# Kernel tuning notes

Measured on AMD Instinct MI355X. Metric: run time of the kernel, lower is better.

The kernel has to match this reference:

```python
import jax, jax.numpy as jnp
import numpy as np

ALPHA = 0.2  # LeakyReLU negative slope


def setup_inputs() -> dict:
    key = jax.random.key(0)
    ks = jax.random.split(key, 7)
    B, Wn, K, E, O = 16, 64, 256, 128, 64
    s = lambda k, shape, fan: jax.random.normal(k, shape, jnp.float32) * (1.0 / np.sqrt(fan))
    return {
        "x": jax.random.normal(ks[0], (B, Wn, K), jnp.float32),
        "lin_w": s(ks[1], (E, 2 * Wn), 2 * Wn),   # torch Linear weight (out,in)
        "lin_b": jnp.zeros((E,), jnp.float32),
        "a": s(ks[2], (E,), E),
        "bias_kk": s(ks[3], (K, K), K) * 0.1,
        "fc_w": s(ks[4], (O, K), K),
        "fc_b": jnp.zeros((O,), jnp.float32),
    }


def reference(x, lin_w, lin_b, a, bias_kk, fc_w, fc_b):
    # x: (B, W, K) -> v: (B, K, W); K nodes, W features per node
    v = jnp.transpose(x, (0, 2, 1))
    Wn = v.shape[-1]
    # lin(concat(v_i, v_j)) == v_i @ W1^T + v_j @ W2^T + b  (avoids O(K^2*2W) concat)
    W1, W2 = lin_w[:, :Wn], lin_w[:, Wn:]
    left = jnp.einsum("bkw,ew->bke", v, W1)   # (B,K,E)
    right = jnp.einsum("bkw,ew->bke", v, W2)  # (B,K,E)
    g = left[:, :, None, :] + right[:, None, :, :] + lin_b  # (B,K,K,E)
    g = jnp.where(g >= 0, g, ALPHA * g)  # LeakyReLU
    e = jnp.einsum("bije,e->bij", g, a) + bias_kk  # (B,K,K)
    attn = jax.nn.softmax(e, axis=2)
    # dropout p=0.0 / eval mode -> identity
    h = jax.nn.sigmoid(jnp.einsum("bij,bjw->biw", attn, v))  # (B,K,W)
    out = jnp.einsum("bwk,ok->bwo", jnp.transpose(h, (0, 2, 1)), fc_w) + fc_b
    return out  # (B, W, out_dim)
```

## Files before the change

kernel.cpp:

```cpp
#include <hip/hip_runtime.h>
#include <hip/hip_bf16.h>

#define ALPHA 0.2f
#define C1 0.6f
#define C2 0.4f

__global__ __launch_bounds__(256) void k_proj(
    const float* __restrict__ x, const float* __restrict__ lin_w,
    float* __restrict__ left, float* __restrict__ right, float* __restrict__ v) {
  const int b  = blockIdx.x >> 5;
  const int k0 = (blockIdx.x & 31) * 8;
  const int tid = threadIdx.x;

  __shared__ float s_x[8][68];

  {
    const int w  = tid >> 2;
    const int kq = tid & 3;
    float2 xv = *(const float2*)(x + b * 16384 + w * 256 + k0 + kq * 2);
    s_x[kq * 2 + 0][w] = xv.x;
    s_x[kq * 2 + 1][w] = xv.y;
  }
  __syncthreads();

  if (tid < 128) {
    const int k  = tid >> 4;
    const int wq = tid & 15;
    float4 vv = *(const float4*)&s_x[k][wq * 4];
    *(float4*)(v + (b * 256 + k0 + k) * 64 + wq * 4) = vv;
  }

  const int e  = tid & 127;
  const int kh = tid >> 7;
  float accL[4] = {0, 0, 0, 0};
  float accR[4] = {0, 0, 0, 0};
  const float4* w1 = (const float4*)(lin_w + e * 128);
  const float4* w2 = w1 + 16;
#pragma unroll
  for (int wc = 0; wc < 16; ++wc) {
    float4 l = w1[wc];
    float4 r = w2[wc];
#pragma unroll
    for (int k = 0; k < 4; ++k) {
      float4 sx = *(const float4*)&s_x[kh * 4 + k][wc * 4];
      accL[k] += sx.x * l.x + sx.y * l.y + sx.z * l.z + sx.w * l.w;
      accR[k] += sx.x * r.x + sx.y * r.y + sx.z * r.z + sx.w * r.w;
    }
  }
#pragma unroll
  for (int k = 0; k < 4; ++k) {
    int kk = (b * 256 + k0 + kh * 4 + k) * 128 + e;
    left[kk]  = accL[k];
    right[kk] = accR[k];
  }
}

__global__ __launch_bounds__(256) void k_attn(
    const float* __restrict__ left, const float* __restrict__ right,
    const float* __restrict__ lin_b, const float* __restrict__ a,
    const float* __restrict__ bias_kk, const float* __restrict__ v,
    float* __restrict__ h) {
  const int b   = blockIdx.x >> 5;
  const int i0  = (blockIdx.x & 31) * 8;
  const int tid = threadIdx.x;

  __shared__ float s_lb[8][132];
  __shared__ float s_a[128];
  __shared__ float s_ca[128];
  __shared__ float s_AL[8];
  __shared__ float s_sc[8][260];
  __shared__ float s_inv[8];
  __shared__ float s_v[128][68];

  float bk[8];
#pragma unroll
  for (int i = 0; i < 8; ++i) bk[i] = bias_kk[(i0 + i) * 256 + tid];

  if (tid < 128) {
    float av = a[tid];
    s_a[tid]  = av;
    s_ca[tid] = C2 * av;
  }
  {
    const int ii = tid >> 5;
    const int e4 = (tid & 31) * 4;
    float4 lv = *(const float4*)(left + (b * 256 + i0 + ii) * 128 + e4);
    float4 bv = *(const float4*)(lin_b + e4);
    lv.x += bv.x; lv.y += bv.y; lv.z += bv.z; lv.w += bv.w;
    *(float4*)&s_lb[ii][e4] = lv;
  }
  __syncthreads();

  {
    const int ii = tid >> 5, sl = tid & 31;
    float p = 0.f;
#pragma unroll
    for (int m = 0; m < 4; ++m) p += s_a[sl * 4 + m] * s_lb[ii][sl * 4 + m];
#pragma unroll
    for (int off = 16; off > 0; off >>= 1) p += __shfl_xor(p, off, 64);
    if (sl == 0) s_AL[ii] = p;
  }

  float acc[8];
#pragma unroll
  for (int i = 0; i < 8; ++i) acc[i] = 0.f;
  float ar = 0.f;
  const float4* rp = (const float4*)(right + (b * 256 + tid) * 128);
#pragma unroll
  for (int ec = 0; ec < 8; ++ec) {
    float4 r0 = rp[ec * 4 + 0], r1 = rp[ec * 4 + 1],
           r2 = rp[ec * 4 + 2], r3 = rp[ec * 4 + 3];
    float4 a0 = *(const float4*)&s_a[ec * 16 + 0];
    float4 a1 = *(const float4*)&s_a[ec * 16 + 4];
    float4 a2 = *(const float4*)&s_a[ec * 16 + 8];
    float4 a3 = *(const float4*)&s_a[ec * 16 + 12];
    ar += a0.x * r0.x + a0.y * r0.y + a0.z * r0.z + a0.w * r0.w;
    ar += a1.x * r1.x + a1.y * r1.y + a1.z * r1.z + a1.w * r1.w;
    ar += a2.x * r2.x + a2.y * r2.y + a2.z * r2.z + a2.w * r2.w;
    ar += a3.x * r3.x + a3.y * r3.y + a3.z * r3.z + a3.w * r3.w;
    float4 c0 = *(const float4*)&s_ca[ec * 16 + 0];
    float4 c1 = *(const float4*)&s_ca[ec * 16 + 4];
    float4 c2 = *(const float4*)&s_ca[ec * 16 + 8];
    float4 c3 = *(const float4*)&s_ca[ec * 16 + 12];
#pragma unroll
    for (int i = 0; i < 8; ++i) {
      float4 l0 = *(const float4*)&s_lb[i][ec * 16 + 0];
      float4 l1 = *(const float4*)&s_lb[i][ec * 16 + 4];
      float4 l2 = *(const float4*)&s_lb[i][ec * 16 + 8];
      float4 l3 = *(const float4*)&s_lb[i][ec * 16 + 12];
      float t, s = acc[i];
      t = l0.x + r0.x; s = fmaf(c0.x, fabsf(t), s);
      t = l0.y + r0.y; s = fmaf(c0.y, fabsf(t), s);
      t = l0.z + r0.z; s = fmaf(c0.z, fabsf(t), s);
      t = l0.w + r0.w; s = fmaf(c0.w, fabsf(t), s);
      t = l1.x + r1.x; s = fmaf(c1.x, fabsf(t), s);
      t = l1.y + r1.y; s = fmaf(c1.y, fabsf(t), s);
      t = l1.z + r1.z; s = fmaf(c1.z, fabsf(t), s);
      t = l1.w + r1.w; s = fmaf(c1.w, fabsf(t), s);
      t = l2.x + r2.x; s = fmaf(c2.x, fabsf(t), s);
      t = l2.y + r2.y; s = fmaf(c2.y, fabsf(t), s);
      t = l2.z + r2.z; s = fmaf(c2.z, fabsf(t), s);
      t = l2.w + r2.w; s = fmaf(c2.w, fabsf(t), s);
      t = l3.x + r3.x; s = fmaf(c3.x, fabsf(t), s);
      t = l3.y + r3.y; s = fmaf(c3.y, fabsf(t), s);
      t = l3.z + r3.z; s = fmaf(c3.z, fabsf(t), s);
      t = l3.w + r3.w; s = fmaf(c3.w, fabsf(t), s);
      acc[i] = s;
    }
  }
  __syncthreads();

#pragma unroll
  for (int i = 0; i < 8; ++i) {
    float sc = fmaf(C1, s_AL[i] + ar, acc[i]) + bk[i];
    s_sc[i][tid] = __expf(sc);
  }
  __syncthreads();

  {
    const int wv = tid >> 6, lane = tid & 63;
#pragma unroll
    for (int rr = 0; rr < 2; ++rr) {
      int i = wv * 2 + rr;
      float s = s_sc[i][lane] + s_sc[i][lane + 64] +
                s_sc[i][lane + 128] + s_sc[i][lane + 192];
#pragma unroll
      for (int off = 32; off > 0; off >>= 1) s += __shfl_xor(s, off, 64);
      if (lane == 0) s_inv[i] = 1.f / s;
    }
  }

  const int iq = tid >> 5;
  const int w  = (tid & 31) * 2;
  float h0 = 0.f, h1 = 0.f;
#pragma unroll
  for (int c = 0; c < 2; ++c) {
    __syncthreads();
#pragma unroll
    for (int t = 0; t < 8; ++t) {
      int idx = tid + t * 256;
      int row = idx >> 4, col = (idx & 15) * 4;
      *(float4*)&s_v[row][col] =
          *(const float4*)(v + (b * 256 + c * 128 + row) * 64 + col);
    }
    __syncthreads();
#pragma unroll 4
    for (int jj = 0; jj < 128; jj += 4) {
      float4 at = *(const float4*)&s_sc[iq][c * 128 + jj];
      float2 v0 = *(const float2*)&s_v[jj + 0][w];
      float2 v1 = *(const float2*)&s_v[jj + 1][w];
      float2 v2 = *(const float2*)&s_v[jj + 2][w];
      float2 v3 = *(const float2*)&s_v[jj + 3][w];
      h0 += at.x * v0.x + at.y * v1.x + at.z * v2.x + at.w * v3.x;
      h1 += at.x * v0.y + at.y * v1.y + at.z * v2.y + at.w * v3.y;
    }
  }
  float inv = s_inv[iq];
  float2 hv;
  hv.x = 1.f / (1.f + __expf(-h0 * inv));
  hv.y = 1.f / (1.f + __expf(-h1 * inv));
  *(float2*)(h + (b * 256 + i0 + iq) * 64 + w) = hv;
}

__global__ __launch_bounds__(256) void k_out(
    const float* __restrict__ h, const float* __restrict__ fc_w,
    const float* __restrict__ fc_b, float* __restrict__ out) {
  const int blk = blockIdx.x;
  const int b   = blk >> 4;
  const int wg  = blk & 15;
  const int wl  = threadIdx.x >> 6;
  const int o   = threadIdx.x & 63;
  const int w   = wg * 4 + wl;

  __shared__ float s_h[256 * 4];
  for (int idx = threadIdx.x; idx < 1024; idx += 256) {
    int k = idx >> 2, wl2 = idx & 3;
    s_h[idx] = h[(b * 256 + k) * 64 + wg * 4 + wl2];
  }
  __syncthreads();

  float acc = 0.f;
  const float4* fw = (const float4*)(fc_w + o * 256);
#pragma unroll
  for (int k4 = 0; k4 < 64; ++k4) {
    float4 f = fw[k4];
    int k = k4 * 4;
    acc += s_h[(k + 0) * 4 + wl] * f.x + s_h[(k + 1) * 4 + wl] * f.y +
           s_h[(k + 2) * 4 + wl] * f.z + s_h[(k + 3) * 4 + wl] * f.w;
  }
  out[b * 64 * 64 + w * 64 + o] = acc + fc_b[o];
}

extern "C" void kernel_launch(void* const* d_in, const int* in_sizes, int n_in,
                              void* d_out, int out_size, void* d_ws, size_t ws_size,
                              hipStream_t stream) {
  const float* x       = (const float*)d_in[0];
  const float* lin_w   = (const float*)d_in[1];
  const float* lin_b   = (const float*)d_in[2];
  const float* a       = (const float*)d_in[3];
  const float* bias_kk = (const float*)d_in[4];
  const float* fc_w    = (const float*)d_in[5];
  const float* fc_b    = (const float*)d_in[6];
  float* out = (float*)d_out;

  float* ws    = (float*)d_ws;
  float* left  = ws;
  float* right = ws + 524288;
  float* v     = ws + 1048576;
  float* h     = ws + 1310720;

  k_proj<<<512, 256, 0, stream>>>(x, lin_w, left, right, v);
  k_attn<<<512, 256, 0, stream>>>(left, right, lin_b, a, bias_kk, v, h);
  k_out<<<256, 256, 0, stream>>>(h, fc_w, fc_b, out);
}
```

Baseline: 106.3 us.

## Fuse three kernels into one cooperative kernel with grid syncs

Merges the projection, attention and output kernels into a single cooperative launch separated by grid-wide barriers. Shared memory is a union across phases, and the V staging tile is halved to 64 rows, with four chunks instead of two, so two blocks can stay resident per CU. This removes two launch gaps and inter-kernel drain, at the cost of grid.sync overhead and the occupancy limits a cooperative launch imposes.

New measurement: 233.1 us. +119.3%, slower.

```diff
diff --git a/kernel.cpp b/kernel.cpp
--- a/kernel.cpp
+++ b/kernel.cpp
@@ -1,234 +1,245 @@
 #include <hip/hip_runtime.h>
 #include <hip/hip_bf16.h>
+#include <hip/hip_cooperative_groups.h>
+
+namespace cg = cooperative_groups;
 
 #define ALPHA 0.2f
 #define C1 0.6f
 #define C2 0.4f
 
-__global__ __launch_bounds__(256) void k_proj(
+struct SA { float x[8][68]; };
+struct SB {
+  float lb[8][132];
+  float a[128];
+  float ca[128];
+  float AL[8];
+  float sc[8][260];
+  float inv[8];
+  float v[64][68];
+};
+struct SC { float h[1024]; };
+union SM { SA pa; SB pb; SC pc; };
+
+__global__ __launch_bounds__(256, 2) void k_fused(
     const float* __restrict__ x, const float* __restrict__ lin_w,
-    float* __restrict__ left, float* __restrict__ right, float* __restrict__ v) {
-  const int b  = blockIdx.x >> 5;
-  const int k0 = (blockIdx.x & 31) * 8;
+    const float* __restrict__ lin_b, const float* __restrict__ a,
+    const float* __restrict__ bias_kk, const float* __restrict__ fc_w,
+    const float* __restrict__ fc_b, float* __restrict__ out,
+    float* __restrict__ left, float* __restrict__ right,
+    float* __restrict__ v, float* __restrict__ h) {
+  cg::grid_group grid = cg::this_grid();
+  __shared__ SM sm;
   const int tid = threadIdx.x;
 
-  __shared__ float s_x[8][68];
-
   {
-    const int w  = tid >> 2;
-    const int kq = tid & 3;
-    float2 xv = *(const float2*)(x + b * 16384 + w * 256 + k0 + kq * 2);
-    s_x[kq * 2 + 0][w] = xv.x;
-    s_x[kq * 2 + 1][w] = xv.y;
+    const int b  = blockIdx.x >> 5;
+    const int k0 = (blockIdx.x & 31) * 8;
+
+    {
+      const int w  = tid >> 2;
+      const int kq = tid & 3;
+      float2 xv = *(const float2*)(x + b * 16384 + w * 256 + k0 + kq * 2);
+      sm.pa.x[kq * 2 + 0][w] = xv.x;
+      sm.pa.x[kq * 2 + 1][w] = xv.y;
+    }
+    __syncthreads();
+
+    if (tid < 128) {
+      const int k  = tid >> 4;
+      const int wq = tid & 15;
+      float4 vv = *(const float4*)&sm.pa.x[k][wq * 4];
+      *(float4*)(v + (b * 256 + k0 + k) * 64 + wq * 4) = vv;
+    }
+
+    const int e  = tid & 127;
+    const int kh = tid >> 7;
+    float accL[4] = {0, 0, 0, 0};
+    float accR[4] = {0, 0, 0, 0};
+    const float4* w1 = (const float4*)(lin_w + e * 128);
+    const float4* w2 = w1 + 16;
+#pragma unroll
+    for (int wc = 0; wc < 16; ++wc) {
+      float4 l = w1[wc];
+      float4 r = w2[wc];
+#pragma unroll
+      for (int k = 0; k < 4; ++k) {
+        float4 sx = *(const float4*)&sm.pa.x[kh * 4 + k][wc * 4];
+        accL[k] += sx.x * l.x + sx.y * l.y + sx.z * l.z + sx.w * l.w;
+        accR[k] += sx.x * r.x + sx.y * r.y + sx.z * r.z + sx.w * r.w;
+      }
+    }
+#pragma unroll
+    for (int k = 0; k < 4; ++k) {
+      int kk = (b * 256 + k0 + kh * 4 + k) * 128 + e;
+      left[kk]  = accL[k];
+      right[kk] = accR[k];
+    }
   }
-  __syncthreads();
-
-  if (tid < 128) {
-    const int k  = tid >> 4;
-    const int wq = tid & 15;
-    float4 vv = *(const float4*)&s_x[k][wq * 4];
-    *(float4*)(v + (b * 256 + k0 + k) * 64 + wq * 4) = vv;
+
+  grid.sync();
+
+  {
+    const int b  = blockIdx.x >> 5;
+    const int i0 = (blockIdx.x & 31) * 8;
+
+    float bk[8];
+#pragma unroll
+    for (int i = 0; i < 8; ++i) bk[i] = bias_kk[(i0 + i) * 256 + tid];
+
+    if (tid < 128) {
+      float av = a[tid];
+      sm.pb.a[tid]  = av;
+      sm.pb.ca[tid] = C2 * av;
+    }
+    {
+      const int ii = tid >> 5;
+      const int e4 = (tid & 31) * 4;
+      float4 lv = *(const float4*)(left + (b * 256 + i0 + ii) * 128 + e4);
+      float4 bv = *(const float4*)(lin_b + e4);
+      lv.x += bv.x; lv.y += bv.y; lv.z += bv.z; lv.w += bv.w;
+      *(float4*)&sm.pb.lb[ii][e4] = lv;
+    }
+    __syncthreads();
+
+    {
+      const int ii = tid >> 5, sl = tid & 31;
+      float p = 0.f;
+#pragma unroll
+      for (int m = 0; m < 4; ++m)
+        p += sm.pb.a[sl * 4 + m] * sm.pb.lb[ii][sl * 4 + m];
+#pragma unroll
+      for (int off = 16; off > 0; off >>= 1) p += __shfl_xor(p, off, 64);
+      if (sl == 0) sm.pb.AL[ii] = p;
+    }
+
+    float acc[8];
+#pragma unroll
+    for (int i = 0; i < 8; ++i) acc[i] = 0.f;
+    float ar = 0.f;
+    const float4* rp = (const float4*)(right + (b * 256 + tid) * 128);
+#pragma unroll
+    for (int ec = 0; ec < 8; ++ec) {
+      float4 r0 = rp[ec * 4 + 0], r1 = rp[ec * 4 + 1],
+             r2 = rp[ec * 4 + 2], r3 = rp[ec * 4 + 3];
+      float4 a0 = *(const float4*)&sm.pb.a[ec * 16 + 0];
+      float4 a1 = *(const float4*)&sm.pb.a[ec * 16 + 4];
+      float4 a2 = *(const float4*)&sm.pb.a[ec * 16 + 8];
+      float4 a3 = *(const float4*)&sm.pb.a[ec * 16 + 12];
+      ar += a0.x * r0.x + a0.y * r0.y + a0.z * r0.z + a0.w * r0.w;
+      ar += a1.x * r1.x + a1.y * r1.y + a1.z * r1.z + a1.w * r1.w;
+      ar += a2.x * r2.x + a2.y * r2.y + a2.z * r2.z + a2.w * r2.w;
+      ar += a3.x * r3.x + a3.y * r3.y + a3.z * r3.z + a3.w * r3.w;
+      float4 c0 = *(const float4*)&sm.pb.ca[ec * 16 + 0];
+      float4 c1 = *(const float4*)&sm.pb.ca[ec * 16 + 4];
+      float4 c2 = *(const float4*)&sm.pb.ca[ec * 16 + 8];
+      float4 c3 = *(const float4*)&sm.pb.ca[ec * 16 + 12];
+#pragma unroll
+      for (int i = 0; i < 8; ++i) {
+        float4 l0 = *(const float4*)&sm.pb.lb[i][ec * 16 + 0];
+        float4 l1 = *(const float4*)&sm.pb.lb[i][ec * 16 + 4];
+        float4 l2 = *(const float4*)&sm.pb.lb[i][ec * 16 + 8];
+        float4 l3 = *(const float4*)&sm.pb.lb[i][ec * 16 + 12];
+        float t, s = acc[i];
+        t = l0.x + r0.x; s = fmaf(c0.x, fabsf(t), s);
+        t = l0.y + r0.y; s = fmaf(c0.y, fabsf(t), s);
+        t = l0.z + r0.z; s = fmaf(c0.z, fabsf(t), s);
+        t = l0.w + r0.w; s = fmaf(c0.w, fabsf(t), s);
+        t = l1.x + r1.x; s = fmaf(c1.x, fabsf(t), s);
+        t = l1.y + r1.y; s = fmaf(c1.y, fabsf(t), s);
+        t = l1.z + r1.z; s = fmaf(c1.z, fabsf(t), s);
+        t = l1.w + r1.w; s = fmaf(c1.w, fabsf(t), s);
+        t = l2.x + r2.x; s = fmaf(c2.x, fabsf(t), s);
+        t = l2.y + r2.y; s = fmaf(c2.y, fabsf(t), s);
+        t = l2.z + r2.z; s = fmaf(c2.z, fabsf(t), s);
+        t = l2.w + r2.w; s = fmaf(c2.w, fabsf(t), s);
+        t = l3.x + r3.x; s = fmaf(c3.x, fabsf(t), s);
+        t = l3.y + r3.y; s = fmaf(c3.y, fabsf(t), s);
+        t = l3.z + r3.z; s = fmaf(c3.z, fabsf(t), s);
+        t = l3.w + r3.w; s = fmaf(c3.w, fabsf(t), s);
+        acc[i] = s;
+      }
+    }
+    __syncthreads();
+
+#pragma unroll
+    for (int i = 0; i < 8; ++i) {
+      float sc = fmaf(C1, sm.pb.AL[i] + ar, acc[i]) + bk[i];
+      sm.pb.sc[i][tid] = __expf(sc);
+    }
+    __syncthreads();
+
+    {
+      const int wv = tid >> 6, lane = tid & 63;
+#pragma unroll
+      for (int rr = 0; rr < 2; ++rr) {
+        int i = wv * 2 + rr;
+        float s = sm.pb.sc[i][lane] + sm.pb.sc[i][lane + 64] +
+                  sm.pb.sc[i][lane + 128] + sm.pb.sc[i][lane + 192];
+#pragma unroll
+        for (int off = 32; off > 0; off >>= 1) s += __shfl_xor(s, off, 64);
+        if (lane == 0) sm.pb.inv[i] = 1.f / s;
+      }
+    }
+
+    const int iq = tid >> 5;
+    const int w  = (tid & 31) * 2;
+    float h0 = 0.f, h1 = 0.f;
+#pragma unroll
+    for (int c = 0; c < 4; ++c) {
+      __syncthreads();
+#pragma unroll
+      for (int t = 0; t < 4; ++t) {
+        int idx = tid + t * 256;
+        int row = idx >> 4, col = (idx & 15) * 4;
+        *(float4*)&sm.pb.v[row][col] =
+            *(const float4*)(v + (b * 256 + c * 64 + row) * 64 + col);
+      }
+      __syncthreads();
+#pragma unroll 4
+      for (int jj = 0; jj < 64; jj += 4) {
+        float4 at = *(const float4*)&sm.pb.sc[iq][c * 64 + jj];
+        float2 v0 = *(const float2*)&sm.pb.v[jj + 0][w];
+        float2 v1 = *(const float2*)&sm.pb.v[jj + 1][w];
+        float2 v2 = *(const float2*)&sm.pb.v[jj + 2][w];
+        float2 v3 = *(const float2*)&sm.pb.v[jj + 3][w];
+        h0 += at.x * v0.x + at.y * v1.x + at.z * v2.x + at.w * v3.x;
+        h1 += at.x * v0.y + at.y * v1.y + at.z * v2.y + at.w * v3.y;
+      }
+    }
+    float inv = sm.pb.inv[iq];
+    float2 hv;
+    hv.x = 1.f / (1.f + __expf(-h0 * inv));
+    hv.y = 1.f / (1.f + __expf(-h1 * inv));
+    *(float2*)(h + (b * 256 + i0 + iq) * 64 + w) = hv;
   }
 
-  const int e  = tid & 127;
-  const int kh = tid >> 7;
-  float accL[4] = {0, 0, 0, 0};
-  float accR[4] = {0, 0, 0, 0};
-  const float4* w1 = (const float4*)(lin_w + e * 128);
-  const float4* w2 = w1 + 16;
-#pragma unroll
-  for (int wc = 0; wc < 16; ++wc) {
-    float4 l = w1[wc];
-    float4 r = w2[wc];
-#pragma unroll
-    for (int k = 0; k < 4; ++k) {
-      float4 sx = *(const float4*)&s_x[kh * 4 + k][wc * 4];
-      accL[k] += sx.x * l.x + sx.y * l.y + sx.z * l.z + sx.w * l.w;
-      accR[k] += sx.x * r.x + sx.y * r.y + sx.z * r.z + sx.w * r.w;
-    }
+  grid.sync();
+
+  if (blockIdx.x < 256) {
+    const int b  = blockIdx.x >> 4;
+    const int wg = blockIdx.x & 15;
+    const int wl = tid >> 6;
+    const int o  = tid & 63;
+    const int w  = wg * 4 + wl;
+
+    for (int idx = tid; idx < 1024; idx += 256) {
+      int k = idx >> 2, wl2 = idx & 3;
+      sm.pc.h[idx] = h[(b * 256 + k) * 64 + wg * 4 + wl2];
+    }
+    __syncthreads();
+
+    float acc = 0.f;
+    const float4* fw = (const float4*)(fc_w + o * 256);
+#pragma unroll
+    for (int k4 = 0; k4 < 64; ++k4) {
+      float4 f = fw[k4];
+      int k = k4 * 4;
+      acc += sm.pc.h[(k + 0) * 4 + wl] * f.x + sm.pc.h[(k + 1) * 4 + wl] * f.y +
+             sm.pc.h[(k + 2) * 4 + wl] * f.z + sm.pc.h[(k + 3) * 4 + wl] * f.w;
+    }
+    out[b * 64 * 64 + w * 64 + o] = acc + fc_b[o];
   }
-#pragma unroll
-  for (int k = 0; k < 4; ++k) {
-    int kk = (b * 256 + k0 + kh * 4 + k) * 128 + e;
-    left[kk]  = accL[k];
-    right[kk] = accR[k];
-  }
-}
-
-__global__ __launch_bounds__(256) void k_attn(
-    const float* __restrict__ left, const float* __restrict__ right,
-    const float* __restrict__ lin_b, const float* __restrict__ a,
-    const float* __restrict__ bias_kk, const float* __restrict__ v,
-    float* __restrict__ h) {
-  const int b   = blockIdx.x >> 5;
-  const int i0  = (blockIdx.x & 31) * 8;
-  const int tid = threadIdx.x;
-
-  __shared__ float s_lb[8][132];
-  __shared__ float s_a[128];
-  __shared__ float s_ca[128];
-  __shared__ float s_AL[8];
-  __shared__ float s_sc[8][260];
-  __shared__ float s_inv[8];
-  __shared__ float s_v[128][68];
-
-  float bk[8];
-#pragma unroll
-  for (int i = 0; i < 8; ++i) bk[i] = bias_kk[(i0 + i) * 256 + tid];
-
-  if (tid < 128) {
-    float av = a[tid];
-    s_a[tid]  = av;
-    s_ca[tid] = C2 * av;
-  }
-  {
-    const int ii = tid >> 5;
-    const int e4 = (tid & 31) * 4;
-    float4 lv = *(const float4*)(left + (b * 256 + i0 + ii) * 128 + e4);
-    float4 bv = *(const float4*)(lin_b + e4);
-    lv.x += bv.x; lv.y += bv.y; lv.z += bv.z; lv.w += bv.w;
-    *(float4*)&s_lb[ii][e4] = lv;
-  }
-  __syncthreads();
-
-  {
-    const int ii = tid >> 5, sl = tid & 31;
-    float p = 0.f;
-#pragma unroll
-    for (int m = 0; m < 4; ++m) p += s_a[sl * 4 + m] * s_lb[ii][sl * 4 + m];
-#pragma unroll
-    for (int off = 16; off > 0; off >>= 1) p += __shfl_xor(p, off, 64);
-    if (sl == 0) s_AL[ii] = p;
-  }
-
-  float acc[8];
-#pragma unroll
-  for (int i = 0; i < 8; ++i) acc[i] = 0.f;
-  float ar = 0.f;
-  const float4* rp = (const float4*)(right + (b * 256 + tid) * 128);
-#pragma unroll
-  for (int ec = 0; ec < 8; ++ec) {
-    float4 r0 = rp[ec * 4 + 0], r1 = rp[ec * 4 + 1],
-           r2 = rp[ec * 4 + 2], r3 = rp[ec * 4 + 3];
-    float4 a0 = *(const float4*)&s_a[ec * 16 + 0];
-    float4 a1 = *(const float4*)&s_a[ec * 16 + 4];
-    float4 a2 = *(const float4*)&s_a[ec * 16 + 8];
-    float4 a3 = *(const float4*)&s_a[ec * 16 + 12];
-    ar += a0.x * r0.x + a0.y * r0.y + a0.z * r0.z + a0.w * r0.w;
-    ar += a1.x * r1.x + a1.y * r1.y + a1.z * r1.z + a1.w * r1.w;
-    ar += a2.x * r2.x + a2.y * r2.y + a2.z * r2.z + a2.w * r2.w;
-    ar += a3.x * r3.x + a3.y * r3.y + a3.z * r3.z + a3.w * r3.w;
-    float4 c0 = *(const float4*)&s_ca[ec * 16 + 0];
-    float4 c1 = *(const float4*)&s_ca[ec * 16 + 4];
-    float4 c2 = *(const float4*)&s_ca[ec * 16 + 8];
-    float4 c3 = *(const float4*)&s_ca[ec * 16 + 12];
-#pragma unroll
-    for (int i = 0; i < 8; ++i) {
-      float4 l0 = *(const float4*)&s_lb[i][ec * 16 + 0];
-      float4 l1 = *(const float4*)&s_lb[i][ec * 16 + 4];
-      float4 l2 = *(const float4*)&s_lb[i][ec * 16 + 8];
-      float4 l3 = *(const float4*)&s_lb[i][ec * 16 + 12];
-      float t, s = acc[i];
-      t = l0.x + r0.x; s = fmaf(c0.x, fabsf(t), s);
-      t = l0.y + r0.y; s = fmaf(c0.y, fabsf(t), s);
-      t = l0.z + r0.z; s = fmaf(c0.z, fabsf(t), s);
-      t = l0.w + r0.w; s = fmaf(c0.w, fabsf(t), s);
-      t = l1.x + r1.x; s = fmaf(c1.x, fabsf(t), s);
-      t = l1.y + r1.y; s = fmaf(c1.y, fabsf(t), s);
-      t = l1.z + r1.z; s = fmaf(c1.z, fabsf(t), s);
-      t = l1.w + r1.w; s = fmaf(c1.w, fabsf(t), s);
-      t = l2.x + r2.x; s = fmaf(c2.x, fabsf(t), s);
-      t = l2.y + r2.y; s = fmaf(c2.y, fabsf(t), s);
-      t = l2.z + r2.z; s = fmaf(c2.z, fabsf(t), s);
-      t = l2.w + r2.w; s = fmaf(c2.w, fabsf(t), s);
-      t = l3.x + r3.x; s = fmaf(c3.x, fabsf(t), s);
-      t = l3.y + r3.y; s = fmaf(c3.y, fabsf(t), s);
-      t = l3.z + r3.z; s = fmaf(c3.z, fabsf(t), s);
-      t = l3.w + r3.w; s = fmaf(c3.w, fabsf(t), s);
-      acc[i] = s;
-    }
-  }
-  __syncthreads();
-
-#pragma unroll
-  for (int i = 0; i < 8; ++i) {
-    float sc = fmaf(C1, s_AL[i] + ar, acc[i]) + bk[i];
-    s_sc[i][tid] = __expf(sc);
-  }
-  __syncthreads();
-
-  {
-    const int wv = tid >> 6, lane = tid & 63;
-#pragma unroll
-    for (int rr = 0; rr < 2; ++rr) {
-      int i = wv * 2 + rr;
-      float s = s_sc[i][lane] + s_sc[i][lane + 64] +
-                s_sc[i][lane + 128] + s_sc[i][lane + 192];
-#pragma unroll
-      for (int off = 32; off > 0; off >>= 1) s += __shfl_xor(s, off, 64);
-      if (lane == 0) s_inv[i] = 1.f / s;
-    }
-  }
-
-  const int iq = tid >> 5;
-  const int w  = (tid & 31) * 2;
-  float h0 = 0.f, h1 = 0.f;
-#pragma unroll
-  for (int c = 0; c < 2; ++c) {
-    __syncthreads();
-#pragma unroll
-    for (int t = 0; t < 8; ++t) {
-      int idx = tid + t * 256;
-      int row = idx >> 4, col = (idx & 15) * 4;
-      *(float4*)&s_v[row][col] =
-          *(const float4*)(v + (b * 256 + c * 128 + row) * 64 + col);
-    }
-    __syncthreads();
-#pragma unroll 4
-    for (int jj = 0; jj < 128; jj += 4) {
-      float4 at = *(const float4*)&s_sc[iq][c * 128 + jj];
-      float2 v0 = *(const float2*)&s_v[jj + 0][w];
-      float2 v1 = *(const float2*)&s_v[jj + 1][w];
-      float2 v2 = *(const float2*)&s_v[jj + 2][w];
-      float2 v3 = *(const float2*)&s_v[jj + 3][w];
-      h0 += at.x * v0.x + at.y * v1.x + at.z * v2.x + at.w * v3.x;
-      h1 += at.x * v0.y + at.y * v1.y + at.z * v2.y + at.w * v3.y;
-    }
-  }
-  float inv = s_inv[iq];
-  float2 hv;
-  hv.x = 1.f / (1.f + __expf(-h0 * inv));
-  hv.y = 1.f / (1.f + __expf(-h1 * inv));
-  *(float2*)(h + (b * 256 + i0 + iq) * 64 + w) = hv;
-}
-
-__global__ __launch_bounds__(256) void k_out(
-    const float* __restrict__ h, const float* __restrict__ fc_w,
-    const float* __restrict__ fc_b, float* __restrict__ out) {
-  const int blk = blockIdx.x;
-  const int b   = blk >> 4;
-  const int wg  = blk & 15;
-  const int wl  = threadIdx.x >> 6;
-  const int o   = threadIdx.x & 63;
-  const int w   = wg * 4 + wl;
-
-  __shared__ float s_h[256 * 4];
-  for (int idx = threadIdx.x; idx < 1024; idx += 256) {
-    int k = idx >> 2, wl2 = idx & 3;
-    s_h[idx] = h[(b * 256 + k) * 64 + wg * 4 + wl2];
-  }
-  __syncthreads();
-
-  float acc = 0.f;
-  const float4* fw = (const float4*)(fc_w + o * 256);
-#pragma unroll
-  for (int k4 = 0; k4 < 64; ++k4) {
-    float4 f = fw[k4];
-    int k = k4 * 4;
-    acc += s_h[(k + 0) * 4 + wl] * f.x + s_h[(k + 1) * 4 + wl] * f.y +
-           s_h[(k + 2) * 4 + wl] * f.z + s_h[(k + 3) * 4 + wl] * f.w;
-  }
-  out[b * 64 * 64 + w * 64 + o] = acc + fc_b[o];
 }
 
 extern "C" void kernel_launch(void* const* d_in, const int* in_sizes, int n_in,
@@ -249,7 +260,10 @@
   float* v     = ws + 1048576;
   float* h     = ws + 1310720;
 
-  k_proj<<<512, 256, 0, stream>>>(x, lin_w, left, right, v);
-  k_attn<<<512, 256, 0, stream>>>(left, right, lin_b, a, bias_kk, v, h);
-  k_out<<<256, 256, 0, stream>>>(h, fc_w, fc_b, out);
+  void* args[] = {
+      (void*)&x, (void*)&lin_w, (void*)&lin_b, (void*)&a, (void*)&bias_kk,
+      (void*)&fc_w, (void*)&fc_b, (void*)&out,
+      (void*)&left, (void*)&right, (void*)&v, (void*)&h};
+  hipLaunchCooperativeKernel((void*)k_fused, dim3(512), dim3(256), args, 0,
+                             stream);
 }
```
